# Optimization experiments

Measured on AMD Instinct MI355X. Metric: run time of the kernel, lower is better.

Reference implementation:

```python
import jax, jax.numpy as jnp
import numpy as np

N = 200000
B = 2
GX, GY, GZ = 480, 360, 32          # full-res voxel grid for input_coords
GX2, GY2, GZ2 = 240, 180, 16       # output_scale grid for bxyz_indx
CIN, CR, COUT = 64, 64, 64
CR2 = CR // 2
P_SCALE = (2, 4, 6, 8)


def setup_inputs() -> dict:
    key = jax.random.key(0)
    ks = jax.random.split(key, 24)
    s = 0.05
    input_data = jax.random.normal(ks[0], (N, CIN), dtype=jnp.float32)
    bcol = jax.random.randint(ks[1], (N, 1), 0, B, dtype=jnp.int32)
    xc = jax.random.randint(ks[2], (N, 1), 0, GX, dtype=jnp.int32)
    yc = jax.random.randint(ks[3], (N, 1), 0, GY, dtype=jnp.int32)
    zc = jax.random.randint(ks[4], (N, 1), 0, GZ, dtype=jnp.int32)
    input_coords = jnp.concatenate([bcol, xc, yc, zc], axis=1)
    input_coords_inv = jax.random.randint(ks[5], (N,), 0, N, dtype=jnp.int32)
    b2 = jax.random.randint(ks[6], (N, 1), 0, B, dtype=jnp.int32)
    x2 = jax.random.randint(ks[7], (N, 1), 0, GX2, dtype=jnp.int32)
    y2 = jax.random.randint(ks[8], (N, 1), 0, GY2, dtype=jnp.int32)
    z2 = jax.random.randint(ks[9], (N, 1), 0, GZ2, dtype=jnp.int32)
    bxyz_indx = jnp.concatenate([b2, x2, y2, z2], axis=1)
    # parameters (torch Linear stored here as [in, out])
    W_red = jax.random.normal(ks[10], (CIN, CR)) * s
    b_red = jnp.zeros((CR,), jnp.float32)
    fc_list_W = jax.random.normal(ks[11], (4, CR, CR2)) * s
    fc_list_b = jnp.zeros((4, CR2), jnp.float32)
    fcs_W = jax.random.normal(ks[12], (4, CR2, CR2)) * s
    fcs_b = jnp.zeros((4, CR2), jnp.float32)
    fc_W = jax.random.normal(ks[13], (CR2, CR2)) * s
    out_fc_W = jax.random.normal(ks[14], (CR2, CR)) * s
    lo_W1 = jax.random.normal(ks[15], (2 * CR, CR)) * s
    lo_W2 = jax.random.normal(ks[16], (CR, COUT)) * s
    lo_b2 = jnp.zeros((COUT,), jnp.float32)
    return dict(input_data=input_data, input_coords=input_coords,
                input_coords_inv=input_coords_inv, bxyz_indx=bxyz_indx,
                W_red=W_red, b_red=b_red, fc_list_W=fc_list_W, fc_list_b=fc_list_b,
                fcs_W=fcs_W, fcs_b=fcs_b, fc_W=fc_W, out_fc_W=out_fc_W,
                lo_W1=lo_W1, lo_W2=lo_W2, lo_b2=lo_b2)


def _segment_mean(x, seg, num_segments):
    sums = jax.ops.segment_sum(x, seg, num_segments=num_segments)
    cnt = jax.ops.segment_sum(jnp.ones((x.shape[0], 1), x.dtype), seg,
                              num_segments=num_segments)
    return sums / jnp.maximum(cnt, 1.0)


def reference(input_data, input_coords, input_coords_inv, bxyz_indx,
              W_red, b_red, fc_list_W, fc_list_b, fcs_W, fcs_b,
              fc_W, out_fc_W, lo_W1, lo_W2, lo_b2):
    reduced = jax.nn.relu(input_data @ W_red + b_red)          # [N, CR]
    bcol = input_coords[:, 0]
    xyz = input_coords[:, 1:]
    outs = []
    for j, ps in enumerate(P_SCALE):
        dx = (GX - 1) // ps + 1
        dy = (GY - 1) // ps + 1
        dz = (GZ - 1) // ps + 1
        q = xyz // ps                                          # [N, 3]
        # dense linearized voxel id replaces torch.unique(return_inverse)
        lin = ((bcol * dx + q[:, 0]) * dy + q[:, 1]) * dz + q[:, 2]
        nseg = B * dx * dy * dz
        fkm = _segment_mean(reduced, lin, nseg)                # [nseg, CR]
        att = jax.nn.relu(fkm @ fc_list_W[j] + fc_list_b[j])   # [nseg, CR2]
        outs.append(att[lin])                                  # gather back [N, CR2]
    scale_features = jnp.stack(outs, axis=1)                   # [N, 4, CR2]
    feat_S = scale_features.sum(axis=1)                        # [N, CR2]
    feat_Z = jax.nn.relu(feat_S @ fc_W)                        # [N, CR2]
    att_v = jax.nn.sigmoid(jnp.einsum('nc,kcd->nkd', feat_Z, fcs_W) + fcs_b)
    fused = (scale_features * att_v).sum(axis=1) @ out_fc_W    # [N, CR]
    output_f = jnp.concatenate([reduced, fused], axis=1)       # [N, 2*CR]
    proj = jax.nn.relu(output_f @ lo_W1) @ lo_W2 + lo_b2       # [N, COUT]
    proj = proj[input_coords_inv]
    # with_fm branch: index = (b, z, y, x) of bxyz_indx (b,x,y,z)
    lin2 = ((bxyz_indx[:, 0] * GZ2 + bxyz_indx[:, 3]) * GY2
            + bxyz_indx[:, 2]) * GX2 + bxyz_indx[:, 1]
    tv_fmap = jax.ops.segment_max(proj, lin2, num_segments=B * GZ2 * GY2 * GX2)
    tv_fmap = jnp.where(jnp.isneginf(tv_fmap), 0.0, tv_fmap)   # empty voxels -> 0
    return proj, tv_fmap, lin2
```

## Files before the change

kernel.cpp:

```cpp
#include <hip/hip_runtime.h>
#include <math.h>

#define NPTS   200000
#define CR     64
#define CR2    32

#define NSEG0      1382400
#define SUM123_ROW2 172800
#define SUM123_ROW3 230400
#define SUM123_ROWS 252000

#define TVSEG  1382400
#define GX2    240
#define GY2    180
#define GZ2    16

#define NBATCH 21600

__device__ __forceinline__ float bcastf(float v, int l) {
    return __int_as_float(__builtin_amdgcn_readlane(__float_as_int(v), l));
}

__device__ __forceinline__ int lin_scale(int b, int x, int y, int z,
                                         int ps, int dx, int dy, int dz) {
    int qx = x / ps, qy = y / ps, qz = z / ps;
    return ((b * dx + qx) * dy + qy) * dz + qz;
}

__device__ __forceinline__ void seg_decode(int seg, int& l1, int& l2, int& l3) {
    int qz = seg & 15; int rest = seg >> 4;
    int qy = rest % 180; int rest2 = rest / 180;
    int qx = rest2 % 240; int bb = rest2 / 240;
    l1 = ((bb * 120 + (qx >> 1)) * 90 + (qy >> 1)) * 8 + (qz >> 1);
    l2 = ((bb *  80 + (qx / 3)) * 60 + (qy / 3)) * 6 + (qz / 3);
    l3 = ((bb *  60 + (qx >> 2)) * 45 + (qy >> 2)) * 4 + (qz >> 2);
}

__global__ __launch_bounds__(256) void k_redscat(
        const float* __restrict__ in, const int* __restrict__ coords,
        const float* __restrict__ Wred, const float* __restrict__ bred,
        float* __restrict__ red, float* __restrict__ sum0,
        float* __restrict__ cnt) {
    __shared__ float Wl[CR * CR];
    for (int i = threadIdx.x; i < CR * CR; i += blockDim.x) Wl[i] = Wred[i];
    __syncthreads();
    int lane = threadIdx.x & 63;
    float bl = bred[lane];
    int wid  = blockIdx.x * 4 + (threadIdx.x >> 6);
    int nw   = gridDim.x * 4;
    for (int p = wid; p < NPTS / 2; p += nw) {
        int r0 = 2 * p, r1 = r0 + 1;
        float x0 = in[(size_t)r0 * CR + lane];
        float x1 = in[(size_t)r1 * CR + lane];
        float acc0 = bl, acc1 = bl;
#pragma unroll
        for (int k = 0; k < CR; ++k) {
            float w = Wl[k * CR + lane];
            acc0 += bcastf(x0, k) * w;
            acc1 += bcastf(x1, k) * w;
        }
        acc0 = fmaxf(acc0, 0.f); acc1 = fmaxf(acc1, 0.f);
        red[(size_t)r0 * CR + lane] = acc0;
        red[(size_t)r1 * CR + lane] = acc1;
        int4 c0 = ((const int4*)coords)[r0];
        int4 c1 = ((const int4*)coords)[r1];
        int l0a = lin_scale(c0.x, c0.y, c0.z, c0.w, 2, 240, 180, 16);
        int l0b = lin_scale(c1.x, c1.y, c1.z, c1.w, 2, 240, 180, 16);
        atomicAdd(&sum0[(size_t)l0a * CR + lane], acc0);
        atomicAdd(&sum0[(size_t)l0b * CR + lane], acc1);
        if (lane == 0) {
            atomicAdd(&cnt[l0a], 1.0f);
            atomicAdd(&cnt[l0b], 1.0f);
        }
    }
}

__global__ __launch_bounds__(256) void k_buildlist(
        const float* __restrict__ cnt, int* __restrict__ list0,
        int* __restrict__ listCount, int* __restrict__ rankArr,
        const float* __restrict__ outW, const float* __restrict__ loW1,
        float* __restrict__ M) {
    if (blockIdx.x >= 270) {
        int e = (blockIdx.x - 270) * 256 + threadIdx.x;
        if (e < 2048) {
            int r = e >> 6, c = e & 63;
            float acc = 0.f;
#pragma unroll
            for (int k = 0; k < 64; ++k)
                acc += outW[r * 64 + k] * loW1[(64 + k) * 64 + c];
            M[e] = acc;
        }
        return;
    }
    __shared__ int s_wavecnt[4];
    __shared__ int s_base;
    int lane = threadIdx.x & 63;
    int w = threadIdx.x >> 6;
    int batch0 = blockIdx.x * 80 + w * 20;
    int mycount = 0;
    for (int b = 0; b < 20; ++b) {
        float c = cnt[(batch0 + b) * 64 + lane];
        unsigned long long mask = __ballot(c > 0.f);
        mycount += __popcll(mask);
    }
    if (lane == 0) s_wavecnt[w] = mycount;
    __syncthreads();
    if (threadIdx.x == 0) {
        int tot = s_wavecnt[0] + s_wavecnt[1] + s_wavecnt[2] + s_wavecnt[3];
        s_base = atomicAdd(listCount, tot);
    }
    __syncthreads();
    int offset = s_base;
    for (int ww = 0; ww < w; ++ww) offset += s_wavecnt[ww];
    for (int b = 0; b < 20; ++b) {
        int cell = (batch0 + b) * 64 + lane;
        float c = cnt[cell];
        unsigned long long mask = __ballot(c > 0.f);
        if (c > 0.f) {
            int my = offset + __popcll(mask & ((1ull << lane) - 1ull));
            list0[my] = cell;
            rankArr[cell] = my;
        }
        offset += __popcll(mask);
    }
}

__global__ __launch_bounds__(256) void k_gatt(
        const float* __restrict__ sum0, float* __restrict__ attbuf,
        const float* __restrict__ cnt,
        const float* __restrict__ fcW, const float* __restrict__ fcB) {
    __shared__ float sw[3 * CR * CR2];
    for (int i = threadIdx.x; i < 3 * CR * CR2; i += blockDim.x)
        sw[i] = fcW[CR * CR2 + i];
    __syncthreads();
    int lane = threadIdx.x & 63;
    int d = lane & 31;
    int wid = blockIdx.x * 4 + (threadIdx.x >> 6);
    int nw  = gridDim.x * 4;
    for (int s = wid; s < SUM123_ROWS; s += nw) {
        int childLin = -1;
        const float* w; float bj;
        if (s < SUM123_ROW2) {
            int qz = s & 7, t = s >> 3;
            int qy = t % 90, t2 = t / 90;
            int qx = t2 % 120, b = t2 / 120;
            if (lane < 8) {
                int i = (lane >> 2) & 1, j = (lane >> 1) & 1, k = lane & 1;
                childLin = ((b * 240 + 2 * qx + i) * 180 + 2 * qy + j) * 16 + 2 * qz + k;
            }
            w = sw; bj = fcB[1 * CR2 + d];
        } else if (s < SUM123_ROW3) {
            int s2 = s - SUM123_ROW2;
            int qz = s2 % 6, t = s2 / 6;
            int qy = t % 60, t2 = t / 60;
            int qx = t2 % 80, b = t2 / 80;
            if (lane < 27) {
                int i = lane / 9, j = (lane / 3) % 3, k = lane % 3;
                int cz = 3 * qz + k;
                if (cz < 16)
                    childLin = ((b * 240 + 3 * qx + i) * 180 + 3 * qy + j) * 16 + cz;
            }
            w = sw + 2048; bj = fcB[2 * CR2 + d];
        } else {
            int s3 = s - SUM123_ROW3;
            int qz = s3 & 3, t = s3 >> 2;
            int qy = t % 45, t2 = t / 45;
            int qx = t2 % 60, b = t2 / 60;
            int i = lane >> 4, j = (lane >> 2) & 3, k = lane & 3;
            childLin = ((b * 240 + 4 * qx + i) * 180 + 4 * qy + j) * 16 + 4 * qz + k;
            w = sw + 4096; bj = fcB[3 * CR2 + d];
        }
        float myc = (childLin >= 0) ? cnt[childLin] : 0.f;
        unsigned long long mask = __ballot(myc > 0.f);
        if (!mask) continue;
        float ctot = myc;
        ctot += __shfl_xor(ctot, 1, 64);
        ctot += __shfl_xor(ctot, 2, 64);
        ctot += __shfl_xor(ctot, 4, 64);
        ctot += __shfl_xor(ctot, 8, 64);
        ctot += __shfl_xor(ctot, 16, 64);
        ctot += __shfl_xor(ctot, 32, 64);
        float acc = 0.f;
        while (mask) {
            int j = __ffsll((long long)mask) - 1; mask &= mask - 1;
            int cl = __builtin_amdgcn_readlane(childLin, j);
            acc += sum0[(size_t)cl * CR + lane];
        }
        float m = acc * (1.f / ctot);
        float p = bj;
#pragma unroll
        for (int k = 0; k < CR; ++k)
            p += bcastf(m, k) * w[k * CR2 + d];
        float att = fmaxf(p, 0.f);
        if (lane < 32) attbuf[(size_t)s * CR2 + lane] = att;
    }
}

__global__ __launch_bounds__(256) void k_segf(
        float* __restrict__ tv, const float* __restrict__ cnt,
        const int* __restrict__ list0, const int* __restrict__ listCount,
        const float* __restrict__ fcW, const float* __restrict__ fcB,
        const float* __restrict__ fc_W, const float* __restrict__ fcsW,
        const float* __restrict__ fcsB, const float* __restrict__ M,
        const float* __restrict__ attbuf, float* __restrict__ gc) {
    __shared__ float s_w0[2048];
    __shared__ float s_fcZ[1024];
    __shared__ float s_fcs[4096];
    __shared__ float s_M[2048];
    for (int i = threadIdx.x; i < 2048; i += 256) s_w0[i]  = fcW[i];
    for (int i = threadIdx.x; i < 1024; i += 256) s_fcZ[i] = fc_W[i];
    for (int i = threadIdx.x; i < 4096; i += 256) s_fcs[i] = fcsW[i];
    for (int i = threadIdx.x; i < 2048; i += 256) s_M[i]   = M[i];
    __syncthreads();

    int lane = threadIdx.x & 63;
    int d = lane & 31;
    int h = lane >> 5;
    float b0  = fcB[d];
    float vbA = fcsB[(h ? 1 : 0) * CR2 + d];
    float vbB = fcsB[(h ? 3 : 2) * CR2 + d];
    const float* VA = s_fcs + (h ? 1 : 0) * 1024;
    const float* VB = s_fcs + (h ? 3 : 2) * 1024;

    int total = listCount[0];
    int ngroups = (total + 3) >> 2;
    int wid = blockIdx.x * 4 + (threadIdx.x >> 6);
    int nw  = gridDim.x * 4;
    for (int g = wid; g < ngroups; g += nw) {
        int r0 = 4 * g;
        int r1 = min(r0 + 1, total - 1);
        int r2 = min(r0 + 2, total - 1);
        int r3 = min(r0 + 3, total - 1);
        int seg0 = list0[r0], seg1 = list0[r1], seg2 = list0[r2], seg3 = list0[r3];
        float* row0 = tv + (size_t)seg0 * CR;
        float* row1 = tv + (size_t)seg1 * CR;
        float* row2 = tv + (size_t)seg2 * CR;
        float* row3 = tv + (size_t)seg3 * CR;
        float m0 = row0[lane] * (1.f / cnt[seg0]);
        float m1 = row1[lane] * (1.f / cnt[seg1]);
        float m2 = row2[lane] * (1.f / cnt[seg2]);
        float m3 = row3[lane] * (1.f / cnt[seg3]);
        row0[lane] = 0.f; row1[lane] = 0.f; row2[lane] = 0.f; row3[lane] = 0.f;

        float p0 = b0, p1 = b0, p2 = b0, p3 = b0;
#pragma unroll
        for (int k = 0; k < CR; ++k) {
            float wk = s_w0[k * CR2 + d];
            p0 += bcastf(m0, k) * wk;
            p1 += bcastf(m1, k) * wk;
            p2 += bcastf(m2, k) * wk;
            p3 += bcastf(m3, k) * wk;
        }
        float a0_0 = fmaxf(p0, 0.f), a0_1 = fmaxf(p1, 0.f);
        float a0_2 = fmaxf(p2, 0.f), a0_3 = fmaxf(p3, 0.f);

        int l1_0, l2_0, l3_0, l1_1, l2_1, l3_1;
        int l1_2, l2_2, l3_2, l1_3, l2_3, l3_3;
        seg_decode(seg0, l1_0, l2_0, l3_0);
        seg_decode(seg1, l1_1, l2_1, l3_1);
        seg_decode(seg2, l1_2, l2_2, l3_2);
        seg_decode(seg3, l1_3, l2_3, l3_3);

        float a1_0 = attbuf[(size_t)l1_0 * CR2 + d];
        float a2_0 = attbuf[(size_t)(SUM123_ROW2 + l2_0) * CR2 + d];
        float a3_0 = attbuf[(size_t)(SUM123_ROW3 + l3_0) * CR2 + d];
        float a1_1 = attbuf[(size_t)l1_1 * CR2 + d];
        float a2_1 = attbuf[(size_t)(SUM123_ROW2 + l2_1) * CR2 + d];
        float a3_1 = attbuf[(size_t)(SUM123_ROW3 + l3_1) * CR2 + d];
        float a1_2 = attbuf[(size_t)l1_2 * CR2 + d];
        float a2_2 = attbuf[(size_t)(SUM123_ROW2 + l2_2) * CR2 + d];
        float a3_2 = attbuf[(size_t)(SUM123_ROW3 + l3_2) * CR2 + d];
        float a1_3 = attbuf[(size_t)l1_3 * CR2 + d];
        float a2_3 = attbuf[(size_t)(SUM123_ROW2 + l2_3) * CR2 + d];
        float a3_3 = attbuf[(size_t)(SUM123_ROW3 + l3_3) * CR2 + d];

        float fS0 = a0_0 + a1_0 + a2_0 + a3_0;
        float fS1 = a0_1 + a1_1 + a2_1 + a3_1;
        float fS2 = a0_2 + a1_2 + a2_2 + a3_2;
        float fS3 = a0_3 + a1_3 + a2_3 + a3_3;

        float z0 = 0.f, z1 = 0.f, z2 = 0.f, z3 = 0.f;
#pragma unroll
        for (int cc = 0; cc < CR2; ++cc) {
            float wz = s_fcZ[cc * CR2 + d];
            z0 += bcastf(fS0, cc) * wz;
            z1 += bcastf(fS1, cc) * wz;
            z2 += bcastf(fS2, cc) * wz;
            z3 += bcastf(fS3, cc) * wz;
        }
        float fZ0 = fmaxf(z0, 0.f), fZ1 = fmaxf(z1, 0.f);
        float fZ2 = fmaxf(z2, 0.f), fZ3 = fmaxf(z3, 0.f);

        float avA0 = vbA, avA1 = vbA, avA2 = vbA, avA3 = vbA;
        float avB0 = vbB, avB1 = vbB, avB2 = vbB, avB3 = vbB;
#pragma unroll
        for (int cc = 0; cc < CR2; ++cc) {
            float wa = VA[cc * CR2 + d];
            float wb = VB[cc * CR2 + d];
            float f0 = bcastf(fZ0, cc), f1 = bcastf(fZ1, cc);
            float f2 = bcastf(fZ2, cc), f3 = bcastf(fZ3, cc);
            avA0 += f0 * wa; avB0 += f0 * wb;
            avA1 += f1 * wa; avB1 += f1 * wb;
            avA2 += f2 * wa; avB2 += f2 * wb;
            avA3 += f3 * wa; avB3 += f3 * wb;
        }
        avA0 = 1.f / (1.f + __expf(-avA0)); avB0 = 1.f / (1.f + __expf(-avB0));
        avA1 = 1.f / (1.f + __expf(-avA1)); avB1 = 1.f / (1.f + __expf(-avB1));
        avA2 = 1.f / (1.f + __expf(-avA2)); avB2 = 1.f / (1.f + __expf(-avB2));
        avA3 = 1.f / (1.f + __expf(-avA3)); avB3 = 1.f / (1.f + __expf(-avB3));

        float u0 = (h ? a1_0 : a0_0) * avA0 + (h ? a3_0 : a2_0) * avB0;
        float u1 = (h ? a1_1 : a0_1) * avA1 + (h ? a3_1 : a2_1) * avB1;
        float u2 = (h ? a1_2 : a0_2) * avA2 + (h ? a3_2 : a2_2) * avB2;
        float u3 = (h ? a1_3 : a0_3) * avA3 + (h ? a3_3 : a2_3) * avB3;
        float fI0 = u0 + __shfl_xor(u0, 32, 64);
        float fI1 = u1 + __shfl_xor(u1, 32, 64);
        float fI2 = u2 + __shfl_xor(u2, 32, 64);
        float fI3 = u3 + __shfl_xor(u3, 32, 64);

        float g0 = 0.f, g1 = 0.f, g2 = 0.f, g3 = 0.f;
#pragma unroll
        for (int dd = 0; dd < CR2; ++dd) {
            float wm = s_M[dd * CR + lane];
            g0 += bcastf(fI0, dd) * wm;
            g1 += bcastf(fI1, dd) * wm;
            g2 += bcastf(fI2, dd) * wm;
            g3 += bcastf(fI3, dd) * wm;
        }
        gc[(size_t)r0 * CR + lane] = g0;
        gc[(size_t)r1 * CR + lane] = g1;
        gc[(size_t)r2 * CR + lane] = g2;
        gc[(size_t)r3 * CR + lane] = g3;
    }
}

__device__ __forceinline__ unsigned int fkey(float f) {
    unsigned int b = __float_as_uint(f);
    return (b & 0x80000000u) ? ~b : (b | 0x80000000u);
}

__global__ __launch_bounds__(256) void k_pgmax(
        const float* __restrict__ red, const float* __restrict__ gc,
        const int* __restrict__ rankArr,
        const int* __restrict__ coords, const int* __restrict__ inv,
        const int* __restrict__ bxyz,
        const float* __restrict__ loW1, const float* __restrict__ loW2,
        const float* __restrict__ lob2, float* __restrict__ outProj,
        float* __restrict__ outLin, unsigned int* __restrict__ tvKey,
        unsigned char* __restrict__ flags) {
    __shared__ float s_W1[4096];
    __shared__ float s_W2[4096];
    for (int i = threadIdx.x; i < 4096; i += 256) s_W1[i] = loW1[i];
    for (int i = threadIdx.x; i < 4096; i += 256) s_W2[i] = loW2[i];
    __syncthreads();

    int lane = threadIdx.x & 63;
    float lob = lob2[lane];
    int wid = blockIdx.x * 4 + (threadIdx.x >> 6);
    int nw  = gridDim.x * 4;
    for (int q = wid; q < NPTS / 4; q += nw) {
        int i0 = 4 * q, i1 = i0 + 1, i2 = i0 + 2, i3 = i0 + 3;
        int s0 = inv[i0], s1 = inv[i1], s2 = inv[i2], s3 = inv[i3];
        int4 c0 = ((const int4*)coords)[s0];
        int4 c1 = ((const int4*)coords)[s1];
        int4 c2 = ((const int4*)coords)[s2];
        int4 c3 = ((const int4*)coords)[s3];
        int l0 = lin_scale(c0.x, c0.y, c0.z, c0.w, 2, 240, 180, 16);
        int l1 = lin_scale(c1.x, c1.y, c1.z, c1.w, 2, 240, 180, 16);
        int l2 = lin_scale(c2.x, c2.y, c2.z, c2.w, 2, 240, 180, 16);
        int l3 = lin_scale(c3.x, c3.y, c3.z, c3.w, 2, 240, 180, 16);
        int rk0 = rankArr[l0], rk1 = rankArr[l1];
        int rk2 = rankArr[l2], rk3 = rankArr[l3];

        float x0 = red[(size_t)s0 * CR + lane];
        float x1 = red[(size_t)s1 * CR + lane];
        float x2 = red[(size_t)s2 * CR + lane];
        float x3 = red[(size_t)s3 * CR + lane];
        float h0 = gc[(size_t)rk0 * CR + lane];
        float h1 = gc[(size_t)rk1 * CR + lane];
        float h2 = gc[(size_t)rk2 * CR + lane];
        float h3 = gc[(size_t)rk3 * CR + lane];
#pragma unroll
        for (int k = 0; k < CR; ++k) {
            float w = s_W1[k * CR + lane];
            h0 += bcastf(x0, k) * w;
            h1 += bcastf(x1, k) * w;
            h2 += bcastf(x2, k) * w;
            h3 += bcastf(x3, k) * w;
        }
        h0 = fmaxf(h0, 0.f); h1 = fmaxf(h1, 0.f);
        h2 = fmaxf(h2, 0.f); h3 = fmaxf(h3, 0.f);

        float q0 = lob, q1 = lob, q2 = lob, q3 = lob;
#pragma unroll
        for (int k = 0; k < CR; ++k) {
            float w = s_W2[k * CR + lane];
            q0 += bcastf(h0, k) * w;
            q1 += bcastf(h1, k) * w;
            q2 += bcastf(h2, k) * w;
            q3 += bcastf(h3, k) * w;
        }
        outProj[(size_t)i0 * CR + lane] = q0;
        outProj[(size_t)i1 * CR + lane] = q1;
        outProj[(size_t)i2 * CR + lane] = q2;
        outProj[(size_t)i3 * CR + lane] = q3;

        int4 b0 = ((const int4*)bxyz)[i0];
        int4 b1 = ((const int4*)bxyz)[i1];
        int4 b2 = ((const int4*)bxyz)[i2];
        int4 b3 = ((const int4*)bxyz)[i3];
        int n0 = ((b0.x * GZ2 + b0.w) * GY2 + b0.z) * GX2 + b0.y;
        int n1 = ((b1.x * GZ2 + b1.w) * GY2 + b1.z) * GX2 + b1.y;
        int n2 = ((b2.x * GZ2 + b2.w) * GY2 + b2.z) * GX2 + b2.y;
        int n3 = ((b3.x * GZ2 + b3.w) * GY2 + b3.z) * GX2 + b3.y;
        if (lane == 0) {
            outLin[i0] = (float)n0; flags[n0] = 1;
            outLin[i1] = (float)n1; flags[n1] = 1;
            outLin[i2] = (float)n2; flags[n2] = 1;
            outLin[i3] = (float)n3; flags[n3] = 1;
        }
        atomicMax(&tvKey[(size_t)n0 * CR + lane], fkey(q0));
        atomicMax(&tvKey[(size_t)n1 * CR + lane], fkey(q1));
        atomicMax(&tvKey[(size_t)n2 * CR + lane], fkey(q2));
        atomicMax(&tvKey[(size_t)n3 * CR + lane], fkey(q3));
    }
}

__global__ __launch_bounds__(256) void k_fix(
        unsigned int* __restrict__ tv, const unsigned char* __restrict__ flags) {
    int lane = threadIdx.x & 63;
    int wid = blockIdx.x * 4 + (threadIdx.x >> 6);
    int nw  = gridDim.x * 4;
    for (int batch = wid; batch < NBATCH; batch += nw) {
        int base = batch * 64;
        unsigned char f = flags[base + lane];
        unsigned long long mask = __ballot(f != 0);
        while (mask) {
            int j = __ffsll((long long)mask) - 1; mask &= mask - 1;
            size_t idx = (size_t)(base + j) * CR + lane;
            unsigned int k = tv[idx];
            float v = (k == 0u) ? 0.f
                    : __uint_as_float((k & 0x80000000u) ? (k & 0x7FFFFFFFu) : ~k);
            ((float*)tv)[idx] = v;
        }
    }
}

extern "C" void kernel_launch(void* const* d_in, const int* in_sizes, int n_in,
                              void* d_out, int out_size, void* d_ws, size_t ws_size,
                              hipStream_t stream) {
    (void)in_sizes; (void)n_in; (void)out_size; (void)ws_size;
    const float* in_data = (const float*)d_in[0];
    const int*   coords  = (const int*)d_in[1];
    const int*   inv     = (const int*)d_in[2];
    const int*   bxyz    = (const int*)d_in[3];
    const float* W_red   = (const float*)d_in[4];
    const float* b_red   = (const float*)d_in[5];
    const float* fcW     = (const float*)d_in[6];
    const float* fcB     = (const float*)d_in[7];
    const float* fcsW    = (const float*)d_in[8];
    const float* fcsB    = (const float*)d_in[9];
    const float* fc_W    = (const float*)d_in[10];
    const float* outW    = (const float*)d_in[11];
    const float* loW1    = (const float*)d_in[12];
    const float* loW2    = (const float*)d_in[13];
    const float* lob2    = (const float*)d_in[14];

    float* outProj = (float*)d_out;
    float* tv      = outProj + (size_t)NPTS * CR;
    float* outLin  = tv + (size_t)TVSEG * CR;

    float* ws_f   = (float*)d_ws;
    float* red    = ws_f;
    float* attbuf = red + (size_t)NPTS * CR;
    float* cnt    = attbuf + (size_t)SUM123_ROWS * CR2;
    int*   listCount = (int*)(cnt + (size_t)NSEG0);
    unsigned char* flags = (unsigned char*)(listCount + 4);
    int*   rankArr   = (int*)(flags + (size_t)TVSEG);
    int*   list0     = rankArr + (size_t)NSEG0;
    float* gc     = (float*)(list0 + (size_t)NPTS);
    float* Mmat   = gc + (size_t)NPTS * CR;

    hipMemsetAsync(tv, 0, (size_t)TVSEG * CR * sizeof(float), stream);
    hipMemsetAsync(cnt, 0, (size_t)NSEG0 * 4 + 16 + (size_t)TVSEG, stream);

    k_redscat<<<2048, 256, 0, stream>>>(in_data, coords, W_red, b_red,
                                        red, tv, cnt);
    k_buildlist<<<278, 256, 0, stream>>>(cnt, list0, listCount, rankArr,
                                         outW, loW1, Mmat);
    k_gatt<<<2048, 256, 0, stream>>>(tv, attbuf, cnt, fcW, fcB);
    k_segf<<<1024, 256, 0, stream>>>(tv, cnt, list0, (const int*)listCount,
                                     fcW, fcB, fc_W, fcsW, fcsB, Mmat,
                                     attbuf, gc);
    k_pgmax<<<2048, 256, 0, stream>>>(red, gc, rankArr, coords, inv, bxyz,
                                      loW1, loW2, lob2, outProj,
                                      outLin, (unsigned int*)tv, flags);
    k_fix<<<1024, 256, 0, stream>>>((unsigned int*)tv, flags);
}
```

Measured before the change: 1.005 ms.

## Process segment pairs per wave in k_gatt and widen grids of several kernels

k_gatt now handles two coarse segments per wave iteration. The two segments share the weight loads in the 64-step matvec, and each half-wave writes one of the two outputs. Buildlist gets four times as many blocks, each scanning fewer cell batches. The segf and fix grids are doubled, launch bounds with a minimum of 4 blocks are added to three kernels, and the pgmax stores are reordered so the bxyz index math runs before the matvecs. These changes aim to raise parallelism and latency hiding, at the cost of register pressure and more divergent gather loops per iteration.

```diff
diff --git a/kernel.cpp b/kernel.cpp
--- a/kernel.cpp
+++ b/kernel.cpp
@@ -34,6 +34,34 @@
     l1 = ((bb * 120 + (qx >> 1)) * 90 + (qy >> 1)) * 8 + (qz >> 1);
     l2 = ((bb *  80 + (qx / 3)) * 60 + (qy / 3)) * 6 + (qz / 3);
     l3 = ((bb *  60 + (qx >> 2)) * 45 + (qy >> 2)) * 4 + (qz >> 2);
+}
+
+__device__ __forceinline__ int gatt_child(int s, int lane) {
+    if (s < SUM123_ROW2) {
+        int qz = s & 7, t = s >> 3;
+        int qy = t % 90, t2 = t / 90;
+        int qx = t2 % 120, b = t2 / 120;
+        if (lane >= 8) return -1;
+        int i = (lane >> 2) & 1, j = (lane >> 1) & 1, k = lane & 1;
+        return ((b * 240 + 2 * qx + i) * 180 + 2 * qy + j) * 16 + 2 * qz + k;
+    } else if (s < SUM123_ROW3) {
+        int s2 = s - SUM123_ROW2;
+        int qz = s2 % 6, t = s2 / 6;
+        int qy = t % 60, t2 = t / 60;
+        int qx = t2 % 80, b = t2 / 80;
+        if (lane >= 27) return -1;
+        int i = lane / 9, j = (lane / 3) % 3, k = lane % 3;
+        int cz = 3 * qz + k;
+        if (cz >= 16) return -1;
+        return ((b * 240 + 3 * qx + i) * 180 + 3 * qy + j) * 16 + cz;
+    } else {
+        int s3 = s - SUM123_ROW3;
+        int qz = s3 & 3, t = s3 >> 2;
+        int qy = t % 45, t2 = t / 45;
+        int qx = t2 % 60, b = t2 / 60;
+        int i = lane >> 4, j = (lane >> 2) & 3, k = lane & 3;
+        return ((b * 240 + 4 * qx + i) * 180 + 4 * qy + j) * 16 + 4 * qz + k;
+    }
 }
 
 __global__ __launch_bounds__(256) void k_redscat(
@@ -80,8 +108,8 @@
         int* __restrict__ listCount, int* __restrict__ rankArr,
         const float* __restrict__ outW, const float* __restrict__ loW1,
         float* __restrict__ M) {
-    if (blockIdx.x >= 270) {
-        int e = (blockIdx.x - 270) * 256 + threadIdx.x;
+    if (blockIdx.x >= 1080) {
+        int e = (blockIdx.x - 1080) * 256 + threadIdx.x;
         if (e < 2048) {
             int r = e >> 6, c = e & 63;
             float acc = 0.f;
@@ -96,9 +124,9 @@
     __shared__ int s_base;
     int lane = threadIdx.x & 63;
     int w = threadIdx.x >> 6;
-    int batch0 = blockIdx.x * 80 + w * 20;
+    int batch0 = blockIdx.x * 20 + w * 5;
     int mycount = 0;
-    for (int b = 0; b < 20; ++b) {
+    for (int b = 0; b < 5; ++b) {
         float c = cnt[(batch0 + b) * 64 + lane];
         unsigned long long mask = __ballot(c > 0.f);
         mycount += __popcll(mask);
@@ -112,7 +140,7 @@
     __syncthreads();
     int offset = s_base;
     for (int ww = 0; ww < w; ++ww) offset += s_wavecnt[ww];
-    for (int b = 0; b < 20; ++b) {
+    for (int b = 0; b < 5; ++b) {
         int cell = (batch0 + b) * 64 + lane;
         float c = cnt[cell];
         unsigned long long mask = __ballot(c > 0.f);
@@ -125,7 +153,7 @@
     }
 }
 
-__global__ __launch_bounds__(256) void k_gatt(
+__global__ __launch_bounds__(256, 4) void k_gatt(
         const float* __restrict__ sum0, float* __restrict__ attbuf,
         const float* __restrict__ cnt,
         const float* __restrict__ fcW, const float* __restrict__ fcB) {
@@ -137,66 +165,52 @@
     int d = lane & 31;
     int wid = blockIdx.x * 4 + (threadIdx.x >> 6);
     int nw  = gridDim.x * 4;
-    for (int s = wid; s < SUM123_ROWS; s += nw) {
-        int childLin = -1;
+    for (int p = wid; p < SUM123_ROWS / 2; p += nw) {
+        int s0 = 2 * p, s1 = s0 + 1;
         const float* w; float bj;
-        if (s < SUM123_ROW2) {
-            int qz = s & 7, t = s >> 3;
-            int qy = t % 90, t2 = t / 90;
-            int qx = t2 % 120, b = t2 / 120;
-            if (lane < 8) {
-                int i = (lane >> 2) & 1, j = (lane >> 1) & 1, k = lane & 1;
-                childLin = ((b * 240 + 2 * qx + i) * 180 + 2 * qy + j) * 16 + 2 * qz + k;
-            }
-            w = sw; bj = fcB[1 * CR2 + d];
-        } else if (s < SUM123_ROW3) {
-            int s2 = s - SUM123_ROW2;
-            int qz = s2 % 6, t = s2 / 6;
-            int qy = t % 60, t2 = t / 60;
-            int qx = t2 % 80, b = t2 / 80;
-            if (lane < 27) {
-                int i = lane / 9, j = (lane / 3) % 3, k = lane % 3;
-                int cz = 3 * qz + k;
-                if (cz < 16)
-                    childLin = ((b * 240 + 3 * qx + i) * 180 + 3 * qy + j) * 16 + cz;
-            }
-            w = sw + 2048; bj = fcB[2 * CR2 + d];
-        } else {
-            int s3 = s - SUM123_ROW3;
-            int qz = s3 & 3, t = s3 >> 2;
-            int qy = t % 45, t2 = t / 45;
-            int qx = t2 % 60, b = t2 / 60;
-            int i = lane >> 4, j = (lane >> 2) & 3, k = lane & 3;
-            childLin = ((b * 240 + 4 * qx + i) * 180 + 4 * qy + j) * 16 + 4 * qz + k;
-            w = sw + 4096; bj = fcB[3 * CR2 + d];
-        }
-        float myc = (childLin >= 0) ? cnt[childLin] : 0.f;
-        unsigned long long mask = __ballot(myc > 0.f);
-        if (!mask) continue;
-        float ctot = myc;
-        ctot += __shfl_xor(ctot, 1, 64);
-        ctot += __shfl_xor(ctot, 2, 64);
-        ctot += __shfl_xor(ctot, 4, 64);
-        ctot += __shfl_xor(ctot, 8, 64);
-        ctot += __shfl_xor(ctot, 16, 64);
-        ctot += __shfl_xor(ctot, 32, 64);
-        float acc = 0.f;
-        while (mask) {
-            int j = __ffsll((long long)mask) - 1; mask &= mask - 1;
-            int cl = __builtin_amdgcn_readlane(childLin, j);
-            acc += sum0[(size_t)cl * CR + lane];
-        }
-        float m = acc * (1.f / ctot);
-        float p = bj;
-#pragma unroll
-        for (int k = 0; k < CR; ++k)
-            p += bcastf(m, k) * w[k * CR2 + d];
-        float att = fmaxf(p, 0.f);
-        if (lane < 32) attbuf[(size_t)s * CR2 + lane] = att;
-    }
-}
-
-__global__ __launch_bounds__(256) void k_segf(
+        if (s0 < SUM123_ROW2)      { w = sw;        bj = fcB[1 * CR2 + d]; }
+        else if (s0 < SUM123_ROW3) { w = sw + 2048; bj = fcB[2 * CR2 + d]; }
+        else                       { w = sw + 4096; bj = fcB[3 * CR2 + d]; }
+        int cl0 = gatt_child(s0, lane);
+        int cl1 = gatt_child(s1, lane);
+        float c0 = (cl0 >= 0) ? cnt[cl0] : 0.f;
+        float c1 = (cl1 >= 0) ? cnt[cl1] : 0.f;
+        unsigned long long mask0 = __ballot(c0 > 0.f);
+        unsigned long long mask1 = __ballot(c1 > 0.f);
+        if (!(mask0 | mask1)) continue;
+        float t0 = c0, t1 = c1;
+#pragma unroll
+        for (int sh = 1; sh <= 32; sh <<= 1) {
+            t0 += __shfl_xor(t0, sh, 64);
+            t1 += __shfl_xor(t1, sh, 64);
+        }
+        float acc0 = 0.f, acc1 = 0.f;
+        while (mask0) {
+            int j = __ffsll((long long)mask0) - 1; mask0 &= mask0 - 1;
+            int cl = __builtin_amdgcn_readlane(cl0, j);
+            acc0 += sum0[(size_t)cl * CR + lane];
+        }
+        while (mask1) {
+            int j = __ffsll((long long)mask1) - 1; mask1 &= mask1 - 1;
+            int cl = __builtin_amdgcn_readlane(cl1, j);
+            acc1 += sum0[(size_t)cl * CR + lane];
+        }
+        float m0 = acc0 * (1.f / fmaxf(t0, 1.f));
+        float m1 = acc1 * (1.f / fmaxf(t1, 1.f));
+        float p0 = bj, p1 = bj;
+#pragma unroll
+        for (int k = 0; k < CR; ++k) {
+            float wk = w[k * CR2 + d];
+            p0 += bcastf(m0, k) * wk;
+            p1 += bcastf(m1, k) * wk;
+        }
+        float a0 = fmaxf(p0, 0.f), a1 = fmaxf(p1, 0.f);
+        if (lane < 32) attbuf[(size_t)s0 * CR2 + lane] = a0;
+        else           attbuf[(size_t)s1 * CR2 + d]    = a1;
+    }
+}
+
+__global__ __launch_bounds__(256, 4) void k_segf(
         float* __restrict__ tv, const float* __restrict__ cnt,
         const int* __restrict__ list0, const int* __restrict__ listCount,
         const float* __restrict__ fcW, const float* __restrict__ fcB,
@@ -339,7 +353,7 @@
     return (b & 0x80000000u) ? ~b : (b | 0x80000000u);
 }
 
-__global__ __launch_bounds__(256) void k_pgmax(
+__global__ __launch_bounds__(256, 4) void k_pgmax(
         const float* __restrict__ red, const float* __restrict__ gc,
         const int* __restrict__ rankArr,
         const int* __restrict__ coords, const int* __restrict__ inv,
@@ -372,39 +386,6 @@
         int rk0 = rankArr[l0], rk1 = rankArr[l1];
         int rk2 = rankArr[l2], rk3 = rankArr[l3];
 
-        float x0 = red[(size_t)s0 * CR + lane];
-        float x1 = red[(size_t)s1 * CR + lane];
-        float x2 = red[(size_t)s2 * CR + lane];
-        float x3 = red[(size_t)s3 * CR + lane];
-        float h0 = gc[(size_t)rk0 * CR + lane];
-        float h1 = gc[(size_t)rk1 * CR + lane];
-        float h2 = gc[(size_t)rk2 * CR + lane];
-        float h3 = gc[(size_t)rk3 * CR + lane];
-#pragma unroll
-        for (int k = 0; k < CR; ++k) {
-            float w = s_W1[k * CR + lane];
-            h0 += bcastf(x0, k) * w;
-            h1 += bcastf(x1, k) * w;
-            h2 += bcastf(x2, k) * w;
-            h3 += bcastf(x3, k) * w;
-        }
-        h0 = fmaxf(h0, 0.f); h1 = fmaxf(h1, 0.f);
-        h2 = fmaxf(h2, 0.f); h3 = fmaxf(h3, 0.f);
-
-        float q0 = lob, q1 = lob, q2 = lob, q3 = lob;
-#pragma unroll
-        for (int k = 0; k < CR; ++k) {
-            float w = s_W2[k * CR + lane];
-            q0 += bcastf(h0, k) * w;
-            q1 += bcastf(h1, k) * w;
-            q2 += bcastf(h2, k) * w;
-            q3 += bcastf(h3, k) * w;
-        }
-        outProj[(size_t)i0 * CR + lane] = q0;
-        outProj[(size_t)i1 * CR + lane] = q1;
-        outProj[(size_t)i2 * CR + lane] = q2;
-        outProj[(size_t)i3 * CR + lane] = q3;
-
         int4 b0 = ((const int4*)bxyz)[i0];
         int4 b1 = ((const int4*)bxyz)[i1];
         int4 b2 = ((const int4*)bxyz)[i2];
@@ -419,6 +400,40 @@
             outLin[i2] = (float)n2; flags[n2] = 1;
             outLin[i3] = (float)n3; flags[n3] = 1;
         }
+
+        float x0 = red[(size_t)s0 * CR + lane];
+        float x1 = red[(size_t)s1 * CR + lane];
+        float x2 = red[(size_t)s2 * CR + lane];
+        float x3 = red[(size_t)s3 * CR + lane];
+        float h0 = gc[(size_t)rk0 * CR + lane];
+        float h1 = gc[(size_t)rk1 * CR + lane];
+        float h2 = gc[(size_t)rk2 * CR + lane];
+        float h3 = gc[(size_t)rk3 * CR + lane];
+#pragma unroll
+        for (int k = 0; k < CR; ++k) {
+            float w = s_W1[k * CR + lane];
+            h0 += bcastf(x0, k) * w;
+            h1 += bcastf(x1, k) * w;
+            h2 += bcastf(x2, k) * w;
+            h3 += bcastf(x3, k) * w;
+        }
+        h0 = fmaxf(h0, 0.f); h1 = fmaxf(h1, 0.f);
+        h2 = fmaxf(h2, 0.f); h3 = fmaxf(h3, 0.f);
+
+        float q0 = lob, q1 = lob, q2 = lob, q3 = lob;
+#pragma unroll
+        for (int k = 0; k < CR; ++k) {
+            float w = s_W2[k * CR + lane];
+            q0 += bcastf(h0, k) * w;
+            q1 += bcastf(h1, k) * w;
+            q2 += bcastf(h2, k) * w;
+            q3 += bcastf(h3, k) * w;
+        }
+        outProj[(size_t)i0 * CR + lane] = q0;
+        outProj[(size_t)i1 * CR + lane] = q1;
+        outProj[(size_t)i2 * CR + lane] = q2;
+        outProj[(size_t)i3 * CR + lane] = q3;
+
         atomicMax(&tvKey[(size_t)n0 * CR + lane], fkey(q0));
         atomicMax(&tvKey[(size_t)n1 * CR + lane], fkey(q1));
         atomicMax(&tvKey[(size_t)n2 * CR + lane], fkey(q2));
@@ -486,14 +501,14 @@
 
     k_redscat<<<2048, 256, 0, stream>>>(in_data, coords, W_red, b_red,
                                         red, tv, cnt);
-    k_buildlist<<<278, 256, 0, stream>>>(cnt, list0, listCount, rankArr,
-                                         outW, loW1, Mmat);
+    k_buildlist<<<1088, 256, 0, stream>>>(cnt, list0, listCount, rankArr,
+                                          outW, loW1, Mmat);
     k_gatt<<<2048, 256, 0, stream>>>(tv, attbuf, cnt, fcW, fcB);
-    k_segf<<<1024, 256, 0, stream>>>(tv, cnt, list0, (const int*)listCount,
+    k_segf<<<2048, 256, 0, stream>>>(tv, cnt, list0, (const int*)listCount,
                                      fcW, fcB, fc_W, fcsW, fcsB, Mmat,
                                      attbuf, gc);
     k_pgmax<<<2048, 256, 0, stream>>>(red, gc, rankArr, coords, inv, bxyz,
                                       loW1, loW2, lob2, outProj,
                                       outLin, (unsigned int*)tv, flags);
-    k_fix<<<1024, 256, 0, stream>>>((unsigned int*)tv, flags);
-}
+    k_fix<<<2048, 256, 0, stream>>>((unsigned int*)tv, flags);
+}
```

After: 2.969 ms. +195.4%, slower.
